# Kernel tuning notes

Hardware: AMD Instinct MI355X
Metric: run time of the kernel (lower is better)

The kernel has to match this reference:

```python
import jax, jax.numpy as jnp
import numpy as np

N_NODES = 100000
N_EDGES = 1600000
IN_CH = 64
HID = 64


def setup_inputs() -> dict:
    key = jax.random.key(0)
    ks = jax.random.split(key, 7)
    x = jax.random.normal(ks[0], (N_NODES, IN_CH), dtype=jnp.float32)
    edge_index = jax.random.randint(ks[1], (2, N_EDGES), 0, N_NODES, dtype=jnp.int64)
    node_pair = jax.random.randint(ks[2], (2,), 0, N_NODES, dtype=jnp.int64)
    W1 = jax.random.normal(ks[3], (IN_CH, HID), dtype=jnp.float32) / np.float32(np.sqrt(IN_CH))
    b1 = jnp.zeros((HID,), dtype=jnp.float32)
    W2 = jax.random.normal(ks[4], (HID, HID), dtype=jnp.float32) / np.float32(np.sqrt(HID))
    b2 = jnp.zeros((HID,), dtype=jnp.float32)
    fc_W = jax.random.normal(ks[5], (2 * HID, 1), dtype=jnp.float32) / np.float32(np.sqrt(2 * HID))
    fc_b = jnp.zeros((1,), dtype=jnp.float32)
    return {"x": x, "edge_index": edge_index, "node_pair": node_pair,
            "W1": W1, "b1": b1, "W2": W2, "b2": b2, "fc_W": fc_W, "fc_b": fc_b}


def gcn_conv(x, W, b, src, dst, n):
    # linear transform then symmetric-normalized scatter-add with self-loops (PyG GCNConv)
    h = x @ W                                   # [n, out]
    loop = jnp.arange(n, dtype=src.dtype)
    s = jnp.concatenate([src, loop])            # [E+n]
    d = jnp.concatenate([dst, loop])
    deg = jax.ops.segment_sum(jnp.ones_like(d, dtype=h.dtype), d, num_segments=n)
    dinv = jnp.where(deg > 0, jax.lax.rsqrt(deg), 0.0)
    norm = dinv[s] * dinv[d]                    # [E+n]
    out = jax.ops.segment_sum(h[s] * norm[:, None], d, num_segments=n)
    return out + b


def reference(x, edge_index, node_pair, W1, b1, W2, b2, fc_W, fc_b):
    src, dst = edge_index[0], edge_index[1]
    n = x.shape[0]
    h = jax.nn.relu(gcn_conv(x, W1, b1, src, dst, n))
    h = jax.nn.relu(gcn_conv(h, W2, b2, src, dst, n))
    z = jnp.concatenate([h[node_pair[0]], h[node_pair[1]]], axis=0)  # [2*HID]
    return jax.nn.sigmoid(z @ fc_W + fc_b)      # [1]
```

## Files before the change

### kernel.cpp

```cpp
#include <hip/hip_runtime.h>
#include <math.h>


#define CH 64
#define E1CAP 4096
#define F1CAP (E1CAP + 2)
#define E2CAP 131072
#define GRID 128
#define BLK 512
#define NWAVE (BLK / 64)
#define NP5 8
#define SPIN_MAX (1 << 20)

struct Params {
    const float* x;
    const int* src; const int* dst; const int* np_;
    const float* W1; const float* b1;
    const float* W2; const float* b2;
    const float* fcW; const float* fcb;
    int* bar;
    int* ctrl;
    int* deg;
    unsigned* bmF1; unsigned* bmNd;
    int* pos1; int* e1s; int* e1d; int* F1;
    int* e2s; int* e2d; float* h1; float* agg1e;
    float* out;
    int E; int N; int bmN;
};

__device__ __forceinline__ float dinv_of(int degv) {
    return rsqrtf((float)(degv + 1));
}

__device__ __forceinline__ void st_agent(int* p, int v) {
    __hip_atomic_store(p, v, __ATOMIC_RELAXED, __HIP_MEMORY_SCOPE_AGENT);
}
__device__ __forceinline__ void st_agent_f(float* p, float v) {
    __hip_atomic_store(p, v, __ATOMIC_RELAXED, __HIP_MEMORY_SCOPE_AGENT);
}
__device__ __forceinline__ int ld_agent(const int* p) {
    return __hip_atomic_load((int*)p, __ATOMIC_RELAXED, __HIP_MEMORY_SCOPE_AGENT);
}
__device__ __forceinline__ unsigned ld_agent_u(const unsigned* p) {
    return __hip_atomic_load((unsigned*)p, __ATOMIC_RELAXED, __HIP_MEMORY_SCOPE_AGENT);
}
__device__ __forceinline__ float ld_agent_f(const float* p) {
    return __hip_atomic_load((float*)p, __ATOMIC_RELAXED, __HIP_MEMORY_SCOPE_AGENT);
}

__device__ __forceinline__ void gbar_arrive(int* bar, int phase) {
    __syncthreads();
    if (threadIdx.x == 0) {
        asm volatile("" ::: "memory");
        st_agent(&bar[blockIdx.x << 4], phase);
    }
}
__device__ __forceinline__ void gbar_wait(int* bar, int phase) {
    if (threadIdx.x < 64) {
        const int l = threadIdx.x;
        for (int it = 0; ; ++it) {
            int a = ld_agent(&bar[l << 4]);
            int b = ld_agent(&bar[(l + 64) << 4]);
            if (__all(min(a, b) >= phase) || it > SPIN_MAX) break;
            __builtin_amdgcn_s_sleep(1);
        }
    }
    __syncthreads();
}
__device__ __forceinline__ void gbar(int* bar, int phase) {
    gbar_arrive(bar, phase);
    gbar_wait(bar, phase);
}

__device__ __forceinline__ void reg_node(int u, unsigned* bmF1, unsigned* bmNd,
                                         int* ctrl, int* F1, int* pos1) {
    unsigned bit = 1u << (u & 31);
    unsigned old = atomicOr(&bmF1[u >> 5], bit);
    if (!(old & bit)) {
        atomicOr(&bmNd[u >> 5], bit);
        int i = atomicAdd(&ctrl[2], 1);
        st_agent(&F1[i], u);
        st_agent(&pos1[u], i);
    }
}

__device__ __forceinline__ void phase_e1f1(int gid, int gsz,
                                           const int* __restrict__ src,
                                           const int* __restrict__ dst, int E,
                                           int p0, int p1, int* ctrl,
                                           int* e1s, int* e1d,
                                           unsigned* bmF1, unsigned* bmNd,
                                           int* F1, int* pos1) {
    if (gid == 0) {
        reg_node(p0, bmF1, bmNd, ctrl, F1, pos1);
        if (p1 != p0) reg_node(p1, bmF1, bmNd, ctrl, F1, pos1);
    }
    const int nvec = E >> 2;
    const int4* dst4 = (const int4*)dst;
    for (int i = gid; i < nvec; i += gsz) {
        int4 d4 = dst4[i];
        int ds[4] = {d4.x, d4.y, d4.z, d4.w};
#pragma unroll
        for (int k = 0; k < 4; k++) {
            int d = ds[k];
            if (d == p0 || d == p1) {
                int s = src[i * 4 + k];
                int idx = atomicAdd(&ctrl[0], 1);
                if (idx < E1CAP) { st_agent(&e1s[idx], s); st_agent(&e1d[idx], d); }
                reg_node(s, bmF1, bmNd, ctrl, F1, pos1);
            }
        }
    }
    for (int e = (nvec << 2) + gid; e < E; e += gsz) {
        int d = dst[e];
        if (d == p0 || d == p1) {
            int s = src[e];
            int idx = atomicAdd(&ctrl[0], 1);
            if (idx < E1CAP) { st_agent(&e1s[idx], s); st_agent(&e1d[idx], d); }
            reg_node(s, bmF1, bmNd, ctrl, F1, pos1);
        }
    }
}

__device__ __forceinline__ void phase_e2(int gid, int gsz,
                                         const int* __restrict__ src,
                                         const int* __restrict__ dst, int E,
                                         const unsigned* __restrict__ bmF1,
                                         unsigned* bmNd, int* ctrl,
                                         int* e2s, int* e2d) {
    const int nvec = E >> 2;
    const int4* dst4 = (const int4*)dst;
    for (int i = gid; i < nvec; i += gsz) {
        int4 d4 = dst4[i];
        int ds[4] = {d4.x, d4.y, d4.z, d4.w};
#pragma unroll
        for (int k = 0; k < 4; k++) {
            int d = ds[k];
            if ((ld_agent_u(&bmF1[d >> 5]) >> (d & 31)) & 1u) {
                int s = src[i * 4 + k];
                atomicOr(&bmNd[s >> 5], 1u << (s & 31));
                int idx = atomicAdd(&ctrl[1], 1);
                if (idx < E2CAP) { st_agent(&e2s[idx], s); st_agent(&e2d[idx], d); }
            }
        }
    }
    for (int e = (nvec << 2) + gid; e < E; e += gsz) {
        int d = dst[e];
        if ((ld_agent_u(&bmF1[d >> 5]) >> (d & 31)) & 1u) {
            int s = src[e];
            atomicOr(&bmNd[s >> 5], 1u << (s & 31));
            int idx = atomicAdd(&ctrl[1], 1);
            if (idx < E2CAP) { st_agent(&e2s[idx], s); st_agent(&e2d[idx], d); }
        }
    }
}

__device__ __forceinline__ void phase_deg(int gid, int gsz,
                                          const int* __restrict__ dst, int E,
                                          const unsigned* __restrict__ bmNd,
                                          int* deg) {
    const int nvec = E >> 2;
    const int4* dst4 = (const int4*)dst;
    for (int i = gid; i < nvec; i += gsz) {
        int4 d4 = dst4[i];
        int ds[4] = {d4.x, d4.y, d4.z, d4.w};
#pragma unroll
        for (int k = 0; k < 4; k++) {
            int d = ds[k];
            if ((ld_agent_u(&bmNd[d >> 5]) >> (d & 31)) & 1u) atomicAdd(&deg[d], 1);
        }
    }
    for (int e = (nvec << 2) + gid; e < E; e += gsz) {
        int d = dst[e];
        if ((ld_agent_u(&bmNd[d >> 5]) >> (d & 31)) & 1u) atomicAdd(&deg[d], 1);
    }
}

__device__ __forceinline__ void phase_agg(int gid, int gsz,
                                          const float* __restrict__ x,
                                          const int* __restrict__ deg,
                                          const int* __restrict__ pos1,
                                          const int* __restrict__ ctrl,
                                          const int* __restrict__ e2s,
                                          const int* __restrict__ e2d,
                                          const int* __restrict__ F1,
                                          float* __restrict__ agg1e) {
    int cnt2 = min(ld_agent(&ctrl[1]), E2CAP);
    int nf1  = min(ld_agent(&ctrl[2]), F1CAP);
    int total = (cnt2 + nf1) << 6;
    for (int idx = gid; idx < total; idx += gsz) {
        int e = idx >> 6, c = idx & 63;
        int row; float val;
        if (e < cnt2) {
            int s = ld_agent(&e2s[e]), u = ld_agent(&e2d[e]);
            float nrm = dinv_of(ld_agent(&deg[s])) * dinv_of(ld_agent(&deg[u]));
            row = ld_agent(&pos1[u]);
            val = nrm * x[(size_t)s * CH + c];
        } else {
            int i = e - cnt2;
            int u = ld_agent(&F1[i]);
            float du = dinv_of(ld_agent(&deg[u]));
            row = i;
            val = du * du * x[(size_t)u * CH + c];
        }
        atomicAdd(&agg1e[row * CH + c], val);
    }
}

__device__ __forceinline__ void phase_h1g(int blockId, int tid,
                                          const float* __restrict__ W1,
                                          const float* __restrict__ b1,
                                          const int* __restrict__ ctrl,
                                          const float* __restrict__ agg1e,
                                          float* __restrict__ h1,
                                          float (*a)[CH]) {
    int nf1 = min(ld_agent(&ctrl[2]), F1CAP);
    int w = tid >> 6, j = tid & 63;
    for (int i = blockId * NWAVE + w; i < nf1; i += NP5 * NWAVE) {
        a[w][j] = ld_agent_f(&agg1e[i * CH + j]);
        float sum = b1[j];
#pragma unroll
        for (int k = 0; k < CH; k++) sum += a[w][k] * W1[k * CH + j];
        st_agent_f(&h1[i * CH + j], fmaxf(sum, 0.f));
    }
}

__device__ __forceinline__ void phase_tail(int tid,
                                           const float* __restrict__ h1,
                                           const int* __restrict__ deg,
                                           const int* __restrict__ pos1,
                                           const int* __restrict__ np_,
                                           const int* __restrict__ ctrl,
                                           const int* __restrict__ e1s,
                                           const int* __restrict__ e1d,
                                           const float* __restrict__ W2,
                                           const float* __restrict__ b2,
                                           const float* __restrict__ fcW,
                                           const float* __restrict__ fcb,
                                           float* __restrict__ out,
                                           float (*a2p)[CH], float (*a2)[CH],
                                           float* partial) {
    int w = tid >> 6, j = tid & 63;
    int t = w >> 2, sub = w & 3;
    int pp = np_[t];
    float dp = dinv_of(ld_agent(&deg[pp]));
    float acc = (sub == 0) ? dp * dp * ld_agent_f(&h1[ld_agent(&pos1[pp]) * CH + j]) : 0.f;
    int cnt1 = min(ld_agent(&ctrl[0]), E1CAP);
    for (int e = sub; e < cnt1; e += 4) {
        if (ld_agent(&e1d[e]) == pp) {
            int s = ld_agent(&e1s[e]);
            acc += dinv_of(ld_agent(&deg[s])) * dp *
                   ld_agent_f(&h1[ld_agent(&pos1[s]) * CH + j]);
        }
    }
    a2p[w][j] = acc;
    __syncthreads();
    if (tid < 128) {
        int t2 = tid >> 6;
        a2[t2][j] = a2p[t2 * 4][j] + a2p[t2 * 4 + 1][j] +
                    a2p[t2 * 4 + 2][j] + a2p[t2 * 4 + 3][j];
    }
    __syncthreads();
    if (tid < 128) {
        int t2 = tid >> 6;
        float sum = b2[j];
#pragma unroll
        for (int k = 0; k < CH; k++) sum += a2[t2][k] * W2[k * CH + j];
        float v = fmaxf(sum, 0.f);
        float pr = v * fcW[t2 * CH + j];
        for (int off = 32; off > 0; off >>= 1) pr += __shfl_down(pr, off);
        if (j == 0) partial[t2] = pr;
    }
    __syncthreads();
    if (tid == 0) {
        float z = partial[0] + partial[1] + fcb[0];
        out[0] = 1.f / (1.f + expf(-z));
    }
}

__global__ __launch_bounds__(BLK, 1) void k_fused(Params p) {
    __shared__ float a[NWAVE][CH];
    __shared__ float a2p[NWAVE][CH];
    __shared__ float a2[2][CH];
    __shared__ float partial[2];
    const int gid = blockIdx.x * BLK + threadIdx.x;
    const int gsz = GRID * BLK;

    phase_e1f1(gid, gsz, p.src, p.dst, p.E, p.np_[0], p.np_[1], p.ctrl,
               p.e1s, p.e1d, p.bmF1, p.bmNd, p.F1, p.pos1);
    gbar(p.bar, 1);
    phase_e2(gid, gsz, p.src, p.dst, p.E, p.bmF1, p.bmNd, p.ctrl, p.e2s, p.e2d);
    gbar(p.bar, 2);
    phase_deg(gid, gsz, p.dst, p.E, p.bmNd, p.deg);
    gbar(p.bar, 3);
    phase_agg(gid, gsz, p.x, p.deg, p.pos1, p.ctrl, p.e2s, p.e2d, p.F1, p.agg1e);
    if (blockIdx.x >= NP5) {
        gbar_arrive(p.bar, 5);
        return;
    }
    gbar(p.bar, 4);
    phase_h1g(blockIdx.x, threadIdx.x, p.W1, p.b1, p.ctrl, p.agg1e, p.h1, a);
    gbar_arrive(p.bar, 5);
    if (blockIdx.x != 0) return;
    gbar_wait(p.bar, 5);
    phase_tail(threadIdx.x, p.h1, p.deg, p.pos1, p.np_, p.ctrl, p.e1s, p.e1d,
               p.W2, p.b2, p.fcW, p.fcb, (float*)p.out, a2p, a2, partial);
}

extern "C" void kernel_launch(void* const* d_in, const int* in_sizes, int n_in,
                              void* d_out, int out_size, void* d_ws, size_t ws_size,
                              hipStream_t stream) {
    const float* x   = (const float*)d_in[0];
    const int*   ei  = (const int*)d_in[1];
    const int*   np_ = (const int*)d_in[2];

    const int N = in_sizes[0] / CH;
    const int E = in_sizes[1] / 2;
    const int bmN = (N + 31) / 32;

    char* w = (char*)d_ws;
    size_t off = 0;
    auto alloc = [&](size_t bytes) {
        size_t o = off;
        off = (off + bytes + 255) & ~((size_t)255);
        return o;
    };
    size_t o_bar  = alloc((size_t)GRID * 16 * 4);
    size_t o_ctrl = alloc(64);
    size_t o_bmF1 = alloc((size_t)bmN * 4);
    size_t o_bmNd = alloc((size_t)bmN * 4);
    size_t o_deg  = alloc((size_t)N * 4);
    size_t o_agg  = alloc((size_t)F1CAP * CH * 4);
    size_t zero_end = off;
    size_t o_pos  = alloc((size_t)N * 4);
    size_t o_e1s  = alloc((size_t)E1CAP * 4);
    size_t o_e1d  = alloc((size_t)E1CAP * 4);
    size_t o_F1   = alloc((size_t)F1CAP * 4);
    size_t o_e2s  = alloc((size_t)E2CAP * 4);
    size_t o_e2d  = alloc((size_t)E2CAP * 4);
    size_t o_h1   = alloc((size_t)F1CAP * CH * 4);
    (void)ws_size;

    Params p;
    p.x    = x;
    p.src  = ei;
    p.dst  = ei + E;
    p.np_  = np_;
    p.W1   = (const float*)d_in[3];
    p.b1   = (const float*)d_in[4];
    p.W2   = (const float*)d_in[5];
    p.b2   = (const float*)d_in[6];
    p.fcW  = (const float*)d_in[7];
    p.fcb  = (const float*)d_in[8];
    p.bar   = (int*)(w + o_bar);
    p.ctrl  = (int*)(w + o_ctrl);
    p.bmF1  = (unsigned*)(w + o_bmF1);
    p.bmNd  = (unsigned*)(w + o_bmNd);
    p.deg   = (int*)(w + o_deg);
    p.agg1e = (float*)(w + o_agg);
    p.pos1  = (int*)(w + o_pos);
    p.e1s   = (int*)(w + o_e1s);
    p.e1d   = (int*)(w + o_e1d);
    p.F1    = (int*)(w + o_F1);
    p.e2s   = (int*)(w + o_e2s);
    p.e2d   = (int*)(w + o_e2d);
    p.h1    = (float*)(w + o_h1);
    p.out  = (float*)d_out;
    p.E = E; p.N = N; p.bmN = bmN;

    (void)hipMemsetAsync(d_ws, 0, zero_end, stream);

    k_fused<<<GRID, BLK, 0, stream>>>(p);
}
```

Before: 132.7 us.

## Cache bitmaps in LDS, pack edge pairs, double grid, batch dst loads

Copies the frontier bitmaps (bmF1, bmNd) into shared memory per block before the e2 and degree scans, replacing agent-scope global atomic loads per edge with LDS reads. Packs src/dst edge lists into single 64-bit entries, doubles the persistent grid to 256 blocks (with the barrier polling 256 slots), and batches four int4 dst loads per thread iteration to raise memory-level parallelism. The costs are a per-block bitmap copy of about 12.5 KB, a larger grid barrier, and more blocks contending on the same counters.

```diff
diff --git a/kernel.cpp b/kernel.cpp
--- a/kernel.cpp
+++ b/kernel.cpp
@@ -6,10 +6,11 @@
 #define E1CAP 4096
 #define F1CAP (E1CAP + 2)
 #define E2CAP 131072
-#define GRID 128
+#define GRID 256
 #define BLK 512
 #define NWAVE (BLK / 64)
 #define NP5 8
+#define BMCAP 3200
 #define SPIN_MAX (1 << 20)
 
 struct Params {
@@ -22,8 +23,8 @@
     int* ctrl;
     int* deg;
     unsigned* bmF1; unsigned* bmNd;
-    int* pos1; int* e1s; int* e1d; int* F1;
-    int* e2s; int* e2d; float* h1; float* agg1e;
+    int* pos1; long long* e1sd; int* F1;
+    long long* e2sd; float* h1; float* agg1e;
     float* out;
     int E; int N; int bmN;
 };
@@ -38,11 +39,14 @@
 __device__ __forceinline__ void st_agent_f(float* p, float v) {
     __hip_atomic_store(p, v, __ATOMIC_RELAXED, __HIP_MEMORY_SCOPE_AGENT);
 }
+__device__ __forceinline__ void st_agent64(long long* p, long long v) {
+    __hip_atomic_store(p, v, __ATOMIC_RELAXED, __HIP_MEMORY_SCOPE_AGENT);
+}
 __device__ __forceinline__ int ld_agent(const int* p) {
     return __hip_atomic_load((int*)p, __ATOMIC_RELAXED, __HIP_MEMORY_SCOPE_AGENT);
 }
-__device__ __forceinline__ unsigned ld_agent_u(const unsigned* p) {
-    return __hip_atomic_load((unsigned*)p, __ATOMIC_RELAXED, __HIP_MEMORY_SCOPE_AGENT);
+__device__ __forceinline__ long long ld_agent64(const long long* p) {
+    return __hip_atomic_load((long long*)p, __ATOMIC_RELAXED, __HIP_MEMORY_SCOPE_AGENT);
 }
 __device__ __forceinline__ float ld_agent_f(const float* p) {
     return __hip_atomic_load((float*)p, __ATOMIC_RELAXED, __HIP_MEMORY_SCOPE_AGENT);
@@ -61,7 +65,9 @@
         for (int it = 0; ; ++it) {
             int a = ld_agent(&bar[l << 4]);
             int b = ld_agent(&bar[(l + 64) << 4]);
-            if (__all(min(a, b) >= phase) || it > SPIN_MAX) break;
+            int c = ld_agent(&bar[(l + 128) << 4]);
+            int d = ld_agent(&bar[(l + 192) << 4]);
+            if (__all(min(min(a, b), min(c, d)) >= phase) || it > SPIN_MAX) break;
             __builtin_amdgcn_s_sleep(1);
         }
     }
@@ -84,11 +90,15 @@
     }
 }
 
+__device__ __forceinline__ long long pack_sd(int s, int d) {
+    return ((long long)(unsigned)d << 32) | (unsigned)s;
+}
+
 __device__ __forceinline__ void phase_e1f1(int gid, int gsz,
                                            const int* __restrict__ src,
                                            const int* __restrict__ dst, int E,
                                            int p0, int p1, int* ctrl,
-                                           int* e1s, int* e1d,
+                                           long long* e1sd,
                                            unsigned* bmF1, unsigned* bmNd,
                                            int* F1, int* pos1) {
     if (gid == 0) {
@@ -97,17 +107,27 @@
     }
     const int nvec = E >> 2;
     const int4* dst4 = (const int4*)dst;
-    for (int i = gid; i < nvec; i += gsz) {
-        int4 d4 = dst4[i];
-        int ds[4] = {d4.x, d4.y, d4.z, d4.w};
-#pragma unroll
-        for (int k = 0; k < 4; k++) {
-            int d = ds[k];
-            if (d == p0 || d == p1) {
-                int s = src[i * 4 + k];
-                int idx = atomicAdd(&ctrl[0], 1);
-                if (idx < E1CAP) { st_agent(&e1s[idx], s); st_agent(&e1d[idx], d); }
-                reg_node(s, bmF1, bmNd, ctrl, F1, pos1);
+    for (int base = gid; base < nvec; base += gsz * 4) {
+        int4 v[4];
+#pragma unroll
+        for (int t = 0; t < 4; t++) {
+            int i = base + t * gsz;
+            if (i < nvec) v[t] = dst4[i];
+        }
+#pragma unroll
+        for (int t = 0; t < 4; t++) {
+            int i = base + t * gsz;
+            if (i >= nvec) continue;
+            int ds[4] = {v[t].x, v[t].y, v[t].z, v[t].w};
+#pragma unroll
+            for (int k = 0; k < 4; k++) {
+                int d = ds[k];
+                if (d == p0 || d == p1) {
+                    int s = src[i * 4 + k];
+                    int idx = atomicAdd(&ctrl[0], 1);
+                    if (idx < E1CAP) st_agent64(&e1sd[idx], pack_sd(s, d));
+                    reg_node(s, bmF1, bmNd, ctrl, F1, pos1);
+                }
             }
         }
     }
@@ -116,63 +136,100 @@
         if (d == p0 || d == p1) {
             int s = src[e];
             int idx = atomicAdd(&ctrl[0], 1);
-            if (idx < E1CAP) { st_agent(&e1s[idx], s); st_agent(&e1d[idx], d); }
+            if (idx < E1CAP) st_agent64(&e1sd[idx], pack_sd(s, d));
             reg_node(s, bmF1, bmNd, ctrl, F1, pos1);
         }
     }
 }
 
-__device__ __forceinline__ void phase_e2(int gid, int gsz,
+__device__ __forceinline__ void phase_e2(int tid, int gid, int gsz,
                                          const int* __restrict__ src,
                                          const int* __restrict__ dst, int E,
                                          const unsigned* __restrict__ bmF1,
                                          unsigned* bmNd, int* ctrl,
-                                         int* e2s, int* e2d) {
+                                         long long* e2sd,
+                                         unsigned* lbm, int bmN) {
+    const bool lds_ok = (bmN <= BMCAP);
+    if (lds_ok)
+        for (int i = tid; i < bmN; i += BLK) lbm[i] = bmF1[i];
+    __syncthreads();
     const int nvec = E >> 2;
     const int4* dst4 = (const int4*)dst;
-    for (int i = gid; i < nvec; i += gsz) {
-        int4 d4 = dst4[i];
-        int ds[4] = {d4.x, d4.y, d4.z, d4.w};
-#pragma unroll
-        for (int k = 0; k < 4; k++) {
-            int d = ds[k];
-            if ((ld_agent_u(&bmF1[d >> 5]) >> (d & 31)) & 1u) {
-                int s = src[i * 4 + k];
-                atomicOr(&bmNd[s >> 5], 1u << (s & 31));
-                int idx = atomicAdd(&ctrl[1], 1);
-                if (idx < E2CAP) { st_agent(&e2s[idx], s); st_agent(&e2d[idx], d); }
+    for (int base = gid; base < nvec; base += gsz * 4) {
+        int4 v[4];
+#pragma unroll
+        for (int t = 0; t < 4; t++) {
+            int i = base + t * gsz;
+            if (i < nvec) v[t] = dst4[i];
+        }
+#pragma unroll
+        for (int t = 0; t < 4; t++) {
+            int i = base + t * gsz;
+            if (i >= nvec) continue;
+            int ds[4] = {v[t].x, v[t].y, v[t].z, v[t].w};
+#pragma unroll
+            for (int k = 0; k < 4; k++) {
+                int d = ds[k];
+                unsigned word;
+                if (lds_ok) word = lbm[d >> 5]; else word = bmF1[d >> 5];
+                if ((word >> (d & 31)) & 1u) {
+                    int s = src[i * 4 + k];
+                    atomicOr(&bmNd[s >> 5], 1u << (s & 31));
+                    int idx = atomicAdd(&ctrl[1], 1);
+                    if (idx < E2CAP) st_agent64(&e2sd[idx], pack_sd(s, d));
+                }
             }
         }
     }
     for (int e = (nvec << 2) + gid; e < E; e += gsz) {
         int d = dst[e];
-        if ((ld_agent_u(&bmF1[d >> 5]) >> (d & 31)) & 1u) {
+        unsigned word;
+        if (lds_ok) word = lbm[d >> 5]; else word = bmF1[d >> 5];
+        if ((word >> (d & 31)) & 1u) {
             int s = src[e];
             atomicOr(&bmNd[s >> 5], 1u << (s & 31));
             int idx = atomicAdd(&ctrl[1], 1);
-            if (idx < E2CAP) { st_agent(&e2s[idx], s); st_agent(&e2d[idx], d); }
-        }
-    }
-}
-
-__device__ __forceinline__ void phase_deg(int gid, int gsz,
+            if (idx < E2CAP) st_agent64(&e2sd[idx], pack_sd(s, d));
+        }
+    }
+}
+
+__device__ __forceinline__ void phase_deg(int tid, int gid, int gsz,
                                           const int* __restrict__ dst, int E,
                                           const unsigned* __restrict__ bmNd,
-                                          int* deg) {
+                                          int* deg, unsigned* lbm, int bmN) {
+    const bool lds_ok = (bmN <= BMCAP);
+    if (lds_ok)
+        for (int i = tid; i < bmN; i += BLK) lbm[i] = bmNd[i];
+    __syncthreads();
     const int nvec = E >> 2;
     const int4* dst4 = (const int4*)dst;
-    for (int i = gid; i < nvec; i += gsz) {
-        int4 d4 = dst4[i];
-        int ds[4] = {d4.x, d4.y, d4.z, d4.w};
-#pragma unroll
-        for (int k = 0; k < 4; k++) {
-            int d = ds[k];
-            if ((ld_agent_u(&bmNd[d >> 5]) >> (d & 31)) & 1u) atomicAdd(&deg[d], 1);
+    for (int base = gid; base < nvec; base += gsz * 4) {
+        int4 v[4];
+#pragma unroll
+        for (int t = 0; t < 4; t++) {
+            int i = base + t * gsz;
+            if (i < nvec) v[t] = dst4[i];
+        }
+#pragma unroll
+        for (int t = 0; t < 4; t++) {
+            int i = base + t * gsz;
+            if (i >= nvec) continue;
+            int ds[4] = {v[t].x, v[t].y, v[t].z, v[t].w};
+#pragma unroll
+            for (int k = 0; k < 4; k++) {
+                int d = ds[k];
+                unsigned word;
+                if (lds_ok) word = lbm[d >> 5]; else word = bmNd[d >> 5];
+                if ((word >> (d & 31)) & 1u) atomicAdd(&deg[d], 1);
+            }
         }
     }
     for (int e = (nvec << 2) + gid; e < E; e += gsz) {
         int d = dst[e];
-        if ((ld_agent_u(&bmNd[d >> 5]) >> (d & 31)) & 1u) atomicAdd(&deg[d], 1);
+        unsigned word;
+        if (lds_ok) word = lbm[d >> 5]; else word = bmNd[d >> 5];
+        if ((word >> (d & 31)) & 1u) atomicAdd(&deg[d], 1);
     }
 }
 
@@ -181,8 +238,7 @@
                                           const int* __restrict__ deg,
                                           const int* __restrict__ pos1,
                                           const int* __restrict__ ctrl,
-                                          const int* __restrict__ e2s,
-                                          const int* __restrict__ e2d,
+                                          const long long* __restrict__ e2sd,
                                           const int* __restrict__ F1,
                                           float* __restrict__ agg1e) {
     int cnt2 = min(ld_agent(&ctrl[1]), E2CAP);
@@ -192,7 +248,8 @@
         int e = idx >> 6, c = idx & 63;
         int row; float val;
         if (e < cnt2) {
-            int s = ld_agent(&e2s[e]), u = ld_agent(&e2d[e]);
+            long long sd = ld_agent64(&e2sd[e]);
+            int s = (int)(sd & 0xffffffffll), u = (int)(sd >> 32);
             float nrm = dinv_of(ld_agent(&deg[s])) * dinv_of(ld_agent(&deg[u]));
             row = ld_agent(&pos1[u]);
             val = nrm * x[(size_t)s * CH + c];
@@ -231,8 +288,7 @@
                                            const int* __restrict__ pos1,
                                            const int* __restrict__ np_,
                                            const int* __restrict__ ctrl,
-                                           const int* __restrict__ e1s,
-                                           const int* __restrict__ e1d,
+                                           const long long* __restrict__ e1sd,
                                            const float* __restrict__ W2,
                                            const float* __restrict__ b2,
                                            const float* __restrict__ fcW,
@@ -244,11 +300,13 @@
     int t = w >> 2, sub = w & 3;
     int pp = np_[t];
     float dp = dinv_of(ld_agent(&deg[pp]));
-    float acc = (sub == 0) ? dp * dp * ld_agent_f(&h1[ld_agent(&pos1[pp]) * CH + j]) : 0.f;
+    float acc = (sub == 0)
+        ? dp * dp * ld_agent_f(&h1[ld_agent(&pos1[pp]) * CH + j]) : 0.f;
     int cnt1 = min(ld_agent(&ctrl[0]), E1CAP);
     for (int e = sub; e < cnt1; e += 4) {
-        if (ld_agent(&e1d[e]) == pp) {
-            int s = ld_agent(&e1s[e]);
+        long long sd = ld_agent64(&e1sd[e]);
+        int s = (int)(sd & 0xffffffffll), d = (int)(sd >> 32);
+        if (d == pp) {
             acc += dinv_of(ld_agent(&deg[s])) * dp *
                    ld_agent_f(&h1[ld_agent(&pos1[s]) * CH + j]);
         }
@@ -279,6 +337,7 @@
 }
 
 __global__ __launch_bounds__(BLK, 1) void k_fused(Params p) {
+    __shared__ unsigned lbm[BMCAP];
     __shared__ float a[NWAVE][CH];
     __shared__ float a2p[NWAVE][CH];
     __shared__ float a2[2][CH];
@@ -287,13 +346,14 @@
     const int gsz = GRID * BLK;
 
     phase_e1f1(gid, gsz, p.src, p.dst, p.E, p.np_[0], p.np_[1], p.ctrl,
-               p.e1s, p.e1d, p.bmF1, p.bmNd, p.F1, p.pos1);
+               p.e1sd, p.bmF1, p.bmNd, p.F1, p.pos1);
     gbar(p.bar, 1);
-    phase_e2(gid, gsz, p.src, p.dst, p.E, p.bmF1, p.bmNd, p.ctrl, p.e2s, p.e2d);
+    phase_e2(threadIdx.x, gid, gsz, p.src, p.dst, p.E, p.bmF1, p.bmNd,
+             p.ctrl, p.e2sd, lbm, p.bmN);
     gbar(p.bar, 2);
-    phase_deg(gid, gsz, p.dst, p.E, p.bmNd, p.deg);
+    phase_deg(threadIdx.x, gid, gsz, p.dst, p.E, p.bmNd, p.deg, lbm, p.bmN);
     gbar(p.bar, 3);
-    phase_agg(gid, gsz, p.x, p.deg, p.pos1, p.ctrl, p.e2s, p.e2d, p.F1, p.agg1e);
+    phase_agg(gid, gsz, p.x, p.deg, p.pos1, p.ctrl, p.e2sd, p.F1, p.agg1e);
     if (blockIdx.x >= NP5) {
         gbar_arrive(p.bar, 5);
         return;
@@ -303,7 +363,7 @@
     gbar_arrive(p.bar, 5);
     if (blockIdx.x != 0) return;
     gbar_wait(p.bar, 5);
-    phase_tail(threadIdx.x, p.h1, p.deg, p.pos1, p.np_, p.ctrl, p.e1s, p.e1d,
+    phase_tail(threadIdx.x, p.h1, p.deg, p.pos1, p.np_, p.ctrl, p.e1sd,
                p.W2, p.b2, p.fcW, p.fcb, (float*)p.out, a2p, a2, partial);
 }
 
@@ -333,11 +393,9 @@
     size_t o_agg  = alloc((size_t)F1CAP * CH * 4);
     size_t zero_end = off;
     size_t o_pos  = alloc((size_t)N * 4);
-    size_t o_e1s  = alloc((size_t)E1CAP * 4);
-    size_t o_e1d  = alloc((size_t)E1CAP * 4);
+    size_t o_e1sd = alloc((size_t)E1CAP * 8);
     size_t o_F1   = alloc((size_t)F1CAP * 4);
-    size_t o_e2s  = alloc((size_t)E2CAP * 4);
-    size_t o_e2d  = alloc((size_t)E2CAP * 4);
+    size_t o_e2sd = alloc((size_t)E2CAP * 8);
     size_t o_h1   = alloc((size_t)F1CAP * CH * 4);
     (void)ws_size;
 
@@ -359,11 +417,9 @@
     p.deg   = (int*)(w + o_deg);
     p.agg1e = (float*)(w + o_agg);
     p.pos1  = (int*)(w + o_pos);
-    p.e1s   = (int*)(w + o_e1s);
-    p.e1d   = (int*)(w + o_e1d);
+    p.e1sd  = (long long*)(w + o_e1sd);
     p.F1    = (int*)(w + o_F1);
-    p.e2s   = (int*)(w + o_e2s);
-    p.e2d   = (int*)(w + o_e2d);
+    p.e2sd  = (long long*)(w + o_e2sd);
     p.h1    = (float*)(w + o_h1);
     p.out  = (float*)d_out;
     p.E = E; p.N = N; p.bmN = bmN;
```

Result: faster. 122.2 us, median of 2 (-7.9%).
